# Optimization experiments

Hardware: AMD Instinct MI355X
Metric: run time of the kernel (lower is better)

The kernel has to match this reference:

```python
import jax, jax.numpy as jnp
import numpy as np
from itertools import combinations

# Static config (mirrors args / init_kwargs)
WAY, SHOT, SEQ_LEN, TSS = 5, 16, 10, 2
DIN, DOUT = 2048, 1152
N_QUERIES = 320
TUPLES = np.array(list(combinations(range(SEQ_LEN), TSS)), dtype=np.int32)  # [T, 2]
T = TUPLES.shape[0]  # 45
S = SHOT * T         # support tuples per class
OTHERS = np.array([[o for o in range(WAY) if o != c] for c in range(WAY)], dtype=np.int32)


def _cdist(a, b):
    # Euclidean distance matrix, [Na, Nb]
    d2 = (jnp.sum(a * a, axis=1)[:, None] + jnp.sum(b * b, axis=1)[None, :]
          - 2.0 * a @ b.T)
    return jnp.sqrt(jnp.maximum(d2, 1e-12))


def setup_inputs() -> dict:
    key = jax.random.key(0)
    k1, k2, k3 = jax.random.split(key, 3)
    support_set = jax.random.normal(k1, (WAY * SHOT, SEQ_LEN, DIN), jnp.float32)
    queries = jax.random.normal(k2, (N_QUERIES, SEQ_LEN, DIN), jnp.float32)
    support_labels = jnp.repeat(jnp.arange(WAY, dtype=jnp.int32), SHOT)
    W = jax.random.normal(k3, (DOUT, DIN * TSS), jnp.float32) / np.sqrt(DIN * TSS)
    b = jnp.zeros((DOUT,), jnp.float32)
    return {"support_set": support_set, "queries": queries,
            "support_labels": support_labels, "W": W, "b": b}


def reference(support_set, queries, support_labels, W, b):
    n_q = queries.shape[0]
    # Build frame-pair tuples: [N, T, TSS*DIN]  (dropout is identity in eval)
    sup_t = support_set[:, TUPLES, :].reshape(support_set.shape[0], T, TSS * DIN)
    q_t = queries[:, TUPLES, :].reshape(n_q, T, TSS * DIN)

    q_emb = jax.nn.relu(q_t.reshape(-1, TSS * DIN) @ W.T + b)          # [n_q*T, DOUT]
    order = jnp.argsort(support_labels).reshape(WAY, SHOT)             # class grouping
    class_sup = sup_t[order].reshape(WAY, S, TSS * DIN)
    sup_emb = jax.nn.relu(class_sup @ W.T + b)                          # [WAY, S, DOUT]

    dist_max_c, ave_all_c, pos_all_c = [], [], []
    for c in range(WAY):
        D = _cdist(q_emb, sup_emb[c])                                   # [n_q*T, S]
        # faithful to torch view(-1, T, shot).topk(k=1,dim=1).mean(dim=1)
        ave = D.reshape(-1, T, SHOT).max(axis=1).mean(axis=1)           # [n_q*T]
        dist_max_c.append(D.max(axis=1).reshape(n_q, T).mean(axis=1))   # [n_q]
        ave_all_c.append(ave)
        pos_all_c.append(jnp.argmax(D, axis=1))                         # [n_q*T]
    dist_max = jnp.stack(dist_max_c, axis=1)                            # [n_q, WAY]

    contrast_c = []
    for c in range(WAY):
        mse = sup_emb[c][pos_all_c[c]]                                  # [n_q*T, DOUT]
        so = sup_emb[OTHERS[c]]                                         # [WAY-1, S, DOUT]
        so_flat = so.reshape(-1, DOUT)
        CD = _cdist(mse, so_flat).reshape(-1, WAY - 1, S).transpose(1, 0, 2)  # [WAY-1, n_q*T, S]
        rec = (CD > ave_all_c[c][None, :, None]).sum(axis=1).astype(jnp.float32)  # [WAY-1, S]
        nz = jnp.maximum((rec > 0).sum(axis=1).astype(jnp.float32), 1.0)
        thr = rec.sum(axis=1) / nz
        mask = (rec < thr[:, None]).astype(jnp.float32).reshape(-1)     # [(WAY-1)*S]
        Dd = _cdist(q_emb, so_flat)                                     # [n_q*T, (WAY-1)*S]
        row = (Dd * mask).sum(axis=1) / jnp.maximum(mask.sum(), 1.0)    # masked mean == mean over gathered cols
        contrast_c.append(row.reshape(n_q, T).mean(axis=1) / (WAY - 1))
    dist_contrast = jnp.stack(contrast_c, axis=1)                       # [n_q, WAY]

    dist_sum = dist_contrast + dist_max
    logits_contrast = dist_max / dist_sum
    # (logits_max, logits_contrast) stacked: [2, n_q, WAY]
    return jnp.stack([dist_max, logits_contrast])
```

## Files before the change

### kernel.cpp

```cpp
#include <hip/hip_runtime.h>
#include <hip/hip_bf16.h>
#include <hip/hip_fp16.h>

#define WAY   5
#define SHOT  16
#define TT    45
#define SS    720
#define NQ    320
#define NQT   14400
#define NS    3600
#define MTOT  18000
#define DIN   2048
#define KDIM  4096
#define DOUT  1152
#define EROWS 18176
#define MAXIT 8192

#define QELT  (NQ * 10 * DIN)
#define SELT  (WAY * SHOT * 10 * DIN)
#define WELT  (DOUT * KDIM)

typedef __attribute__((ext_vector_type(8))) short bf16x8;
typedef __attribute__((ext_vector_type(8))) unsigned short u16x8;
typedef __attribute__((ext_vector_type(4))) float f32x4;

#define AS1 __attribute__((address_space(1)))
#define AS3 __attribute__((address_space(3)))

__constant__ unsigned char TUPI[TT] = {
  0,0,0,0,0,0,0,0,0, 1,1,1,1,1,1,1,1, 2,2,2,2,2,2,2,
  3,3,3,3,3,3, 4,4,4,4,4, 5,5,5,5, 6,6,6, 7,7, 8};
__constant__ unsigned char TUPJ[TT] = {
  1,2,3,4,5,6,7,8,9, 2,3,4,5,6,7,8,9, 3,4,5,6,7,8,9,
  4,5,6,7,8,9, 5,6,7,8,9, 6,7,8,9, 7,8,9, 8,9, 9};

__device__ inline unsigned short f2bf(float f) {
  union { float f; unsigned u; } v; v.f = f;
  unsigned r = v.u + 0x7FFFu + ((v.u >> 16) & 1u);
  return (unsigned short)(r >> 16);
}
__device__ inline float bf2f(unsigned short b) {
  union { unsigned u; float f; } v; v.u = ((unsigned)b) << 16;
  return v.f;
}
__device__ inline float h2f(unsigned short h) {
  union { __half h; unsigned short u; } v; v.u = h;
  return __half2float(v.h);
}
__device__ inline unsigned short f2h(float f) {
  union { __half h; unsigned short u; } v; v.h = __float2half(f);
  return v.u;
}

__device__ inline int xcd_swz(int o, int nwg) {
  int q = nwg >> 3, r = nwg & 7;
  int x = o & 7, i = o >> 3;
  return (x < r ? x * (q + 1) : r * (q + 1) + (x - r) * q) + i;
}

__global__ void sentinelK(float* __restrict__ out, float v) {
  int i = blockIdx.x * 256 + threadIdx.x;
  if (i < 2 * NQ * WAY) out[i] = v;
}

__global__ void packK(const float* __restrict__ qry, const float* __restrict__ sup,
                      const float* __restrict__ Wsrc,
                      unsigned short* __restrict__ qbf, unsigned short* __restrict__ sbf,
                      unsigned short* __restrict__ Wbf) {
  long long e = ((long long)blockIdx.x * 256 + threadIdx.x) * 8;
  const float* src; unsigned short* dst; long long o;
  if (e < QELT)                { src = qry;  dst = qbf; o = e; }
  else if (e < QELT + SELT)    { src = sup;  dst = sbf; o = e - QELT; }
  else if (e < QELT + SELT + WELT) { src = Wsrc; dst = Wbf; o = e - QELT - SELT; }
  else return;
  float4 a = *(const float4*)(src + o);
  float4 b = *(const float4*)(src + o + 4);
  u16x8 v;
  v[0] = f2bf(a.x); v[1] = f2bf(a.y); v[2] = f2bf(a.z); v[3] = f2bf(a.w);
  v[4] = f2bf(b.x); v[5] = f2bf(b.y); v[6] = f2bf(b.z); v[7] = f2bf(b.w);
  *(u16x8*)(dst + o) = v;
}

__global__ __launch_bounds__(256) void gemm1K(
    const unsigned short* __restrict__ qbf, const unsigned short* __restrict__ sbf,
    const unsigned short* __restrict__ Wbf, const float* __restrict__ bias,
    unsigned short* __restrict__ emb) {
  __shared__ unsigned short smem[16384];
  unsigned short* Alds = smem;
  unsigned short* Blds = smem + 8192;
  const int tid = threadIdx.x;
  const int lane = tid & 63;
  const int w = tid >> 6, wr = w >> 1, wc = w & 1;
  const int wg = xcd_swz(blockIdx.x, 141 * 9);
  const int bm = wg / 9, bn = wg % 9;

  const unsigned short* pAI[4];
  const unsigned short* pAJ[4];
  const unsigned short* pB[4];
  int ldso[4];
  const int cg8 = ((lane & 7) ^ (lane >> 3)) * 8;
  const unsigned short* Bbase = Wbf + (size_t)bn * 128 * KDIM;
#pragma unroll
  for (int i = 0; i < 4; ++i) {
    int row = w * 32 + i * 8 + (lane >> 3);
    int gr = bm * 128 + row;
    const unsigned short* base; int t;
    if (gr < NQT)       { t = gr % TT; base = qbf + (size_t)(gr / TT) * (10 * DIN); }
    else if (gr < MTOT) { int u = gr - NQT; int c = u / SS; int s = u % SS; t = s % TT;
                          base = sbf + (size_t)(c * SHOT + s / TT) * (10 * DIN); }
    else                { t = 0; base = qbf; }
    pAI[i] = base + (int)TUPI[t] * DIN + cg8;
    pAJ[i] = base + (int)TUPJ[t] * DIN + cg8;
    pB[i]  = Bbase + (size_t)row * KDIM + cg8;
    ldso[i] = __builtin_amdgcn_readfirstlane((w * 32 + i * 8) * 64);
  }
  const int l7 = lane & 7, c2b = lane >> 4;
  const int fo0 = (c2b ^ l7) << 3, fo1 = ((4 | c2b) ^ l7) << 3;
  int aoff[4], boff[4];
#pragma unroll
  for (int m = 0; m < 4; ++m) aoff[m] = (wr * 64 + m * 16 + (lane & 15)) * 64;
#pragma unroll
  for (int n = 0; n < 4; ++n) boff[n] = (wc * 64 + n * 16 + (lane & 15)) * 64;

  f32x4 acc[4][4] = {};

#pragma unroll
  for (int half = 0; half < 2; ++half) {
    const unsigned short* pA0 = half ? pAJ[0] : pAI[0];
    const unsigned short* pA1 = half ? pAJ[1] : pAI[1];
    const unsigned short* pA2 = half ? pAJ[2] : pAI[2];
    const unsigned short* pA3 = half ? pAJ[3] : pAI[3];
    for (int kt2 = 0; kt2 < 32; ++kt2) {
      __builtin_amdgcn_global_load_lds((const AS1 void*)pA0, (AS3 void*)(Alds + ldso[0]), 16, 0, 0); pA0 += 64;
      __builtin_amdgcn_global_load_lds((const AS1 void*)pA1, (AS3 void*)(Alds + ldso[1]), 16, 0, 0); pA1 += 64;
      __builtin_amdgcn_global_load_lds((const AS1 void*)pA2, (AS3 void*)(Alds + ldso[2]), 16, 0, 0); pA2 += 64;
      __builtin_amdgcn_global_load_lds((const AS1 void*)pA3, (AS3 void*)(Alds + ldso[3]), 16, 0, 0); pA3 += 64;
      __builtin_amdgcn_global_load_lds((const AS1 void*)pB[0], (AS3 void*)(Blds + ldso[0]), 16, 0, 0); pB[0] += 64;
      __builtin_amdgcn_global_load_lds((const AS1 void*)pB[1], (AS3 void*)(Blds + ldso[1]), 16, 0, 0); pB[1] += 64;
      __builtin_amdgcn_global_load_lds((const AS1 void*)pB[2], (AS3 void*)(Blds + ldso[2]), 16, 0, 0); pB[2] += 64;
      __builtin_amdgcn_global_load_lds((const AS1 void*)pB[3], (AS3 void*)(Blds + ldso[3]), 16, 0, 0); pB[3] += 64;
      __syncthreads();
#pragma unroll
      for (int kk = 0; kk < 2; ++kk) {
        const int fo = kk ? fo1 : fo0;
        bf16x8 af[4], bfr[4];
#pragma unroll
        for (int m = 0; m < 4; ++m) af[m] = *(const bf16x8*)(&Alds[aoff[m] + fo]);
#pragma unroll
        for (int n = 0; n < 4; ++n) bfr[n] = *(const bf16x8*)(&Blds[boff[n] + fo]);
#pragma unroll
        for (int m = 0; m < 4; ++m)
#pragma unroll
          for (int n = 0; n < 4; ++n)
            acc[m][n] = __builtin_amdgcn_mfma_f32_16x16x32_bf16(af[m], bfr[n], acc[m][n], 0, 0, 0);
      }
      __syncthreads();
    }
  }

  const int lr0 = (lane >> 4) * 4;
  const int lc = lane & 15;
#pragma unroll
  for (int m = 0; m < 4; ++m)
#pragma unroll
    for (int n = 0; n < 4; ++n) {
      int lcol = wc * 64 + n * 16 + lc;
      float bv = bias[bn * 128 + lcol];
#pragma unroll
      for (int q = 0; q < 4; ++q) {
        int lrow = wr * 64 + m * 16 + lr0 + q;
        smem[lrow * 128 + (lcol ^ (((lrow >> 2) & 7) << 4))] =
            f2bf(fmaxf(acc[m][n][q] + bv, 0.0f));
      }
    }
  __syncthreads();
#pragma unroll
  for (int u8i = 0; u8i < 8; ++u8i) {
    int u = u8i * 256 + tid;
    int row = u >> 4, ch = u & 15;
    int gr = bm * 128 + row;
    if (gr < MTOT) {
      u16x8 v = *(const u16x8*)(&smem[row * 128 + ((ch * 8) ^ (((row >> 2) & 7) << 4))]);
      *(u16x8*)(&emb[(size_t)gr * DOUT + bn * 128 + ch * 8]) = v;
    }
  }
}

__global__ __launch_bounds__(256) void gemm2K(
    const unsigned short* __restrict__ emb, const float* __restrict__ norms,
    __half* __restrict__ Dh) {
  __shared__ unsigned short smem[16384];
  unsigned short* Alds = smem;
  unsigned short* Blds = smem + 8192;
  const int tid = threadIdx.x;
  const int lane = tid & 63;
  const int w = tid >> 6, wr = w >> 1, wc = w & 1;
  const int wg = xcd_swz(blockIdx.x, 141 * 29);
  const int bm = wg / 29, bn = wg % 29;

  const unsigned short* pA[4];
  const unsigned short* pB[4];
  int ldso[4];
  const int cg8 = ((lane & 7) ^ (lane >> 3)) * 8;
  const unsigned short* Abase = emb + (size_t)bm * 128 * DOUT;
  const unsigned short* Bbase = emb + (size_t)(NQT + bn * 128) * DOUT;
#pragma unroll
  for (int i = 0; i < 4; ++i) {
    int row = w * 32 + i * 8 + (lane >> 3);
    pA[i] = Abase + (size_t)row * DOUT + cg8;
    pB[i] = Bbase + (size_t)row * DOUT + cg8;
    ldso[i] = __builtin_amdgcn_readfirstlane((w * 32 + i * 8) * 64);
  }
  const int l7 = lane & 7, c2b = lane >> 4;
  const int fo0 = (c2b ^ l7) << 3, fo1 = ((4 | c2b) ^ l7) << 3;
  int aoff[4], boff[4];
#pragma unroll
  for (int m = 0; m < 4; ++m) aoff[m] = (wr * 64 + m * 16 + (lane & 15)) * 64;
#pragma unroll
  for (int n = 0; n < 4; ++n) boff[n] = (wc * 64 + n * 16 + (lane & 15)) * 64;

  f32x4 acc[4][4] = {};

  for (int kt = 0; kt < DOUT / 64; ++kt) {
    __builtin_amdgcn_global_load_lds((const AS1 void*)pA[0], (AS3 void*)(Alds + ldso[0]), 16, 0, 0); pA[0] += 64;
    __builtin_amdgcn_global_load_lds((const AS1 void*)pA[1], (AS3 void*)(Alds + ldso[1]), 16, 0, 0); pA[1] += 64;
    __builtin_amdgcn_global_load_lds((const AS1 void*)pA[2], (AS3 void*)(Alds + ldso[2]), 16, 0, 0); pA[2] += 64;
    __builtin_amdgcn_global_load_lds((const AS1 void*)pA[3], (AS3 void*)(Alds + ldso[3]), 16, 0, 0); pA[3] += 64;
    __builtin_amdgcn_global_load_lds((const AS1 void*)pB[0], (AS3 void*)(Blds + ldso[0]), 16, 0, 0); pB[0] += 64;
    __builtin_amdgcn_global_load_lds((const AS1 void*)pB[1], (AS3 void*)(Blds + ldso[1]), 16, 0, 0); pB[1] += 64;
    __builtin_amdgcn_global_load_lds((const AS1 void*)pB[2], (AS3 void*)(Blds + ldso[2]), 16, 0, 0); pB[2] += 64;
    __builtin_amdgcn_global_load_lds((const AS1 void*)pB[3], (AS3 void*)(Blds + ldso[3]), 16, 0, 0); pB[3] += 64;
    __syncthreads();
#pragma unroll
    for (int kk = 0; kk < 2; ++kk) {
      const int fo = kk ? fo1 : fo0;
      bf16x8 af[4], bfr[4];
#pragma unroll
      for (int m = 0; m < 4; ++m) af[m] = *(const bf16x8*)(&Alds[aoff[m] + fo]);
#pragma unroll
      for (int n = 0; n < 4; ++n) bfr[n] = *(const bf16x8*)(&Blds[boff[n] + fo]);
#pragma unroll
      for (int m = 0; m < 4; ++m)
#pragma unroll
        for (int n = 0; n < 4; ++n)
          acc[m][n] = __builtin_amdgcn_mfma_f32_16x16x32_bf16(af[m], bfr[n], acc[m][n], 0, 0, 0);
    }
    __syncthreads();
  }

  const int lr0 = (lane >> 4) * 4;
  const int lc = lane & 15;
#pragma unroll
  for (int m = 0; m < 4; ++m)
#pragma unroll
    for (int n = 0; n < 4; ++n) {
      int lcol = wc * 64 + n * 16 + lc;
      float nb_ = norms[NQT + bn * 128 + lcol];
#pragma unroll
      for (int q = 0; q < 4; ++q) {
        int lrow = wr * 64 + m * 16 + lr0 + q;
        float d2 = norms[bm * 128 + lrow] + nb_ - 2.0f * acc[m][n][q];
        smem[lrow * 128 + (lcol ^ (((lrow >> 2) & 7) << 4))] =
            f2h(sqrtf(fmaxf(d2, 1e-12f)));
      }
    }
  __syncthreads();
  unsigned short* Dhu = (unsigned short*)Dh;
#pragma unroll
  for (int u8i = 0; u8i < 8; ++u8i) {
    int u = u8i * 256 + tid;
    int row = u >> 4, ch = u & 15;
    int gr = bm * 128 + row;
    int gc0 = bn * 128 + ch * 8;
    if (gr < MTOT && gc0 < NS) {
      u16x8 v = *(const u16x8*)(&smem[row * 128 + ((ch * 8) ^ (((row >> 2) & 7) << 4))]);
      *(u16x8*)(&Dhu[(size_t)gr * NS + gc0]) = v;
    }
  }
}

__global__ void normK(const unsigned short* __restrict__ emb, float* __restrict__ norms) {
  int row = blockIdx.x * 4 + (threadIdx.x >> 6);
  int lane = threadIdx.x & 63;
  const unsigned short* e = emb + (size_t)row * DOUT;
  float acc = 0.f;
  u16x8 x0 = *(const u16x8*)(e + lane * 8);
  u16x8 x1 = *(const u16x8*)(e + 512 + lane * 8);
#pragma unroll
  for (int k = 0; k < 8; ++k) {
    float a = bf2f(x0[k]); acc += a * a;
    float b = bf2f(x1[k]); acc += b * b;
  }
  unsigned t = *(const unsigned*)(e + 1024 + lane * 2);
  float c0 = bf2f((unsigned short)(t & 0xFFFFu)); acc += c0 * c0;
  float c1 = bf2f((unsigned short)(t >> 16));     acc += c1 * c1;
  for (int sh = 1; sh < 64; sh <<= 1) acc += __shfl_xor(acc, sh);
  if (lane == 0) norms[row] = acc;
}

__global__ void passA(const __half* __restrict__ Dh, float* __restrict__ rowmax,
                      float* __restrict__ ave, int* __restrict__ pos) {
  int wid = blockIdx.x * 4 + (threadIdx.x >> 6);
  int lane = threadIdx.x & 63;
  int c = wid / NQT, r = wid % NQT;
  const unsigned short* row = (const unsigned short*)(Dh + (size_t)r * NS + c * SS);
  u16x8 v0 = *(const u16x8*)(row + lane * 8);
  bool act1 = lane < 26;
  u16x8 v1 = v0;
  if (act1) v1 = *(const u16x8*)(row + 512 + lane * 8);
  float m8[8];
  unsigned pm = 0;
#pragma unroll
  for (int k = 0; k < 8; ++k) {
    unsigned h0 = v0[k];
    int col0 = lane * 8 + k;
    unsigned p0 = (h0 << 16) | (unsigned)(65535 - col0);
    pm = pm > p0 ? pm : p0;
    m8[k] = h2f((unsigned short)h0);
  }
  if (act1) {
#pragma unroll
    for (int k = 0; k < 8; ++k) {
      unsigned h1 = v1[k];
      int col1 = 512 + lane * 8 + k;
      unsigned p1 = (h1 << 16) | (unsigned)(65535 - col1);
      pm = pm > p1 ? pm : p1;
      m8[k] = fmaxf(m8[k], h2f((unsigned short)h1));
    }
  }
  for (int sh = 1; sh < 64; sh <<= 1) {
    unsigned o = (unsigned)__shfl_xor((int)pm, sh);
    pm = pm > o ? pm : o;
  }
  for (int sh = 2; sh < 64; sh <<= 1) {
#pragma unroll
    for (int k = 0; k < 8; ++k)
      m8[k] = fmaxf(m8[k], __shfl_xor(m8[k], sh));
  }
  float sj = ((m8[0] + m8[1]) + (m8[2] + m8[3])) + ((m8[4] + m8[5]) + (m8[6] + m8[7]));
  sj += __shfl_xor(sj, 1);
  if (lane == 0) {
    rowmax[c * NQT + r] = h2f((unsigned short)(pm >> 16));
    ave[c * NQT + r] = sj * (1.0f / 16.0f);
    pos[c * NQT + r] = 65535 - (int)(pm & 0xFFFFu);
  }
}

__global__ void bucketCntK(const int* __restrict__ pos, unsigned* __restrict__ bcnt) {
  __shared__ unsigned h[NS];
  int tid = threadIdx.x;
  for (int i = tid; i < NS; i += 256) h[i] = 0;
  __syncthreads();
  for (int idx = blockIdx.x * 256 + tid; idx < WAY * NQT; idx += gridDim.x * 256) {
    int c = idx / NQT;
    atomicAdd(&h[c * SS + pos[idx]], 1u);
  }
  __syncthreads();
  for (int i = tid; i < NS; i += 256) {
    unsigned v = h[i];
    if (v) atomicAdd(&bcnt[i], v);
  }
}

__global__ void pfxItemsK(const unsigned* __restrict__ bcnt, unsigned* __restrict__ bstart,
                          unsigned* __restrict__ nitems, unsigned* __restrict__ items) {
  __shared__ unsigned s[1024];
  int c = blockIdx.x, tid = threadIdx.x;
  for (int i = tid; i < 1024; i += 256) s[i] = (i < SS) ? bcnt[c * SS + i] : 0u;
  __syncthreads();
  for (int off = 1; off < 1024; off <<= 1) {
    unsigned v[4];
#pragma unroll
    for (int k = 0; k < 4; ++k) { int i = tid + k * 256; v[k] = (i >= off) ? s[i - off] : 0u; }
    __syncthreads();
#pragma unroll
    for (int k = 0; k < 4; ++k) { int i = tid + k * 256; s[i] += v[k]; }
    __syncthreads();
  }
  for (int i = tid; i < SS; i += 256) {
    unsigned excl = (i ? s[i - 1] : 0u);
    bstart[c * SS + i] = excl;
    unsigned nb = s[i] - excl;
    if (nb) {
      unsigned ni = (nb + 63) >> 6;
      unsigned base = atomicAdd(nitems, ni);
      for (unsigned k = 0; k < ni; ++k) items[base + k] = ((unsigned)(c * SS + i) << 8) | k;
    }
  }
}

__global__ void bucketSctK(const int* __restrict__ pos, const float* __restrict__ ave,
                           const unsigned* __restrict__ bstart, unsigned* __restrict__ bfill,
                           float* __restrict__ bav) {
  int idx = blockIdx.x * 256 + threadIdx.x;
  if (idx >= WAY * NQT) return;
  int c = idx / NQT;
  int p = pos[idx];
  unsigned j = atomicAdd(&bfill[c * SS + p], 1u);
  bav[c * NQT + bstart[c * SS + p] + j] = ave[idx];
}

__global__ __launch_bounds__(256) void recK4(const __half* __restrict__ Dh,
                                             const unsigned* __restrict__ bstart,
                                             const unsigned* __restrict__ bcnt,
                                             const float* __restrict__ bav,
                                             const unsigned* __restrict__ items,
                                             const unsigned* __restrict__ nitems,
                                             unsigned* __restrict__ rec) {
  int lane = threadIdx.x & 63, wv = threadIdx.x >> 6;
  int nit = (int)nitems[0];
  int nw = gridDim.x * 4;
  for (int i = blockIdx.x * 4 + wv; i < nit; i += nw) {
    unsigned it = items[i];
    int cp = (int)(it >> 8), k = (int)(it & 255u);
    int c = cp / SS, p = cp % SS;
    int c0 = c * SS;
    int b0 = (int)bstart[cp], nb = (int)bcnt[cp];
    int j0 = k << 6;
    float av = (j0 + lane < nb) ? bav[c * NQT + b0 + j0 + lane] : 3.0e38f;
    const __half* row = Dh + (size_t)(NQT + c0 + p) * NS;
    for (int itr = 0; itr < 45; ++itr) {
      int os = itr * 64 + lane;
      int col = os + ((os >= c0) ? SS : 0);
      float v = __half2float(row[col]);
      unsigned cnt = 0;
#pragma unroll 16
      for (int j = 0; j < 64; ++j)
        cnt += (v > __shfl(av, j)) ? 1u : 0u;
      if (cnt) atomicAdd(&rec[c * 2880 + os], cnt);
    }
  }
}

__global__ void maskK(const unsigned* __restrict__ rec, float* __restrict__ maskfull,
                      float* __restrict__ nmask) {
  int c = blockIdx.x;
  int tid = threadIdx.x, lane = tid & 63, wv = tid >> 6;
  __shared__ float thr[WAY - 1];
  __shared__ float red[8];
  for (int o = 0; o < WAY - 1; ++o) {
    float s = 0.f, nz = 0.f;
    for (int i = tid; i < SS; i += 256) {
      unsigned v = rec[c * (WAY - 1) * SS + o * SS + i];
      s += (float)v;
      if (v > 0u) nz += 1.f;
    }
    for (int sh = 1; sh < 64; sh <<= 1) { s += __shfl_xor(s, sh); nz += __shfl_xor(nz, sh); }
    if (lane == 0) { red[wv] = s; red[4 + wv] = nz; }
    __syncthreads();
    if (tid == 0) thr[o] = (red[0] + red[1] + red[2] + red[3]) /
                           fmaxf(red[4] + red[5] + red[6] + red[7], 1.0f);
    __syncthreads();
  }
  float cntm = 0.f;
  for (int col = tid; col < NS; col += 256) {
    float mv = 0.f;
    int cb = col / SS;
    if (cb != c) {
      int os = col - ((col >= (c + 1) * SS) ? SS : 0);
      mv = (((float)rec[c * (WAY - 1) * SS + os]) < thr[os / SS]) ? 1.f : 0.f;
    }
    maskfull[c * NS + col] = mv;
    cntm += mv;
  }
  for (int sh = 1; sh < 64; sh <<= 1) cntm += __shfl_xor(cntm, sh);
  if (lane == 0) red[wv] = cntm;
  __syncthreads();
  if (tid == 0) nmask[c] = red[0] + red[1] + red[2] + red[3];
}

__global__ void mask5K(const float* __restrict__ maskfull, unsigned char* __restrict__ mask5) {
  int col = blockIdx.x * 256 + threadIdx.x;
  if (col >= NS) return;
  unsigned m = 0;
#pragma unroll
  for (int c = 0; c < WAY; ++c)
    m |= (maskfull[c * NS + col] > 0.5f) ? (1u << c) : 0u;
  mask5[col] = (unsigned char)m;
}

__global__ void passB(const __half* __restrict__ Dh, const unsigned char* __restrict__ mask5,
                      const float* __restrict__ nmask, float* __restrict__ row5) {
  int r = blockIdx.x * 4 + (threadIdx.x >> 6);
  int lane = threadIdx.x & 63;
  const unsigned short* drow = (const unsigned short*)(Dh + (size_t)r * NS);
  float a[WAY] = {0.f, 0.f, 0.f, 0.f, 0.f};
#pragma unroll
  for (int it = 0; it < 8; ++it) {
    int col = it * 512 + lane * 8;
    if (col < NS) {
      u16x8 v = *(const u16x8*)(drow + col);
      unsigned long long mb = *(const unsigned long long*)(mask5 + col);
#pragma unroll
      for (int k = 0; k < 8; ++k) {
        float f = h2f(v[k]);
        unsigned m = (unsigned)(mb >> (8 * k)) & 31u;
#pragma unroll
        for (int c = 0; c < WAY; ++c) a[c] += ((m >> c) & 1u) ? f : 0.f;
      }
    }
  }
#pragma unroll
  for (int c = 0; c < WAY; ++c)
    for (int sh = 1; sh < 64; sh <<= 1) a[c] += __shfl_xor(a[c], sh);
  if (lane == 0)
#pragma unroll
    for (int c = 0; c < WAY; ++c)
      row5[(size_t)r * WAY + c] = a[c] / fmaxf(nmask[c], 1.0f);
}

__global__ void finalK(const float* __restrict__ rowmax, const float* __restrict__ row5,
                       float* __restrict__ out) {
  int idx = blockIdx.x * 256 + threadIdx.x;
  if (idx >= NQ * WAY) return;
  int q = idx / WAY, c = idx % WAY;
  float sm = 0.f, sc = 0.f;
  for (int t = 0; t < TT; ++t) {
    int r = q * TT + t;
    sm += rowmax[c * NQT + r];
    sc += row5[(size_t)r * WAY + c];
  }
  float dm = sm / 45.0f;
  float ctr = sc / 45.0f * 0.25f;
  out[idx] = dm;
  out[NQ * WAY + idx] = dm / (ctr + dm);
}

extern "C" void kernel_launch(void* const* d_in, const int* in_sizes, int n_in,
                              void* d_out, int out_size, void* d_ws, size_t ws_size,
                              hipStream_t stream) {
  const float* sup  = (const float*)d_in[0];
  const float* qry  = (const float*)d_in[1];
  const float* Wsrc = (const float*)d_in[3];
  const float* bias = (const float*)d_in[4];
  float* out = (float*)d_out;

  char* base = (char*)d_ws;
  size_t off = 0;
  __half* Dh = (__half*)(base + off);                  off += (size_t)MTOT * NS * 2;
  unsigned short* qbf = (unsigned short*)Dh;
  unsigned short* sbf = qbf + QELT;
  unsigned short* Wbf = sbf + SELT;
  unsigned short* emb = (unsigned short*)(base + off); off += (size_t)EROWS * DOUT * 2;
  float* norms  = (float*)(base + off);   off += (size_t)EROWS * 4;
  float* rowmax = (float*)(base + off);   off += (size_t)WAY * NQT * 4;
  float* ave    = (float*)(base + off);   off += (size_t)WAY * NQT * 4;
  int*   pos    = (int*)(base + off);     off += (size_t)WAY * NQT * 4;
  char* zbase = base + off;
  unsigned* rec    = (unsigned*)(base + off); off += (size_t)WAY * (WAY - 1) * SS * 4;
  unsigned* bcnt   = (unsigned*)(base + off); off += (size_t)WAY * SS * 4;
  unsigned* bfill  = (unsigned*)(base + off); off += (size_t)WAY * SS * 4;
  unsigned* nitems = (unsigned*)(base + off); off += 64;
  size_t zbytes = (size_t)((base + off) - zbase);
  unsigned* bstart = (unsigned*)(base + off); off += (size_t)WAY * SS * 4;
  float* maskfull = (float*)(base + off); off += (size_t)WAY * NS * 4;
  unsigned char* mask5 = (unsigned char*)(base + off); off += 4096;
  float* nmask  = (float*)(base + off);   off += 64;
  float* row5   = (float*)(base + off);   off += (size_t)NQT * WAY * 4;
  float* bav    = (float*)(base + off);   off += (size_t)WAY * NQT * 4;
  unsigned* items = (unsigned*)(base + off); off += MAXIT * 4;

  if (ws_size < off) {
    sentinelK<<<13, 256, 0, stream>>>(out, -(1000.0f + (float)(ws_size >> 20)));
    return;
  }

  (void)hipMemsetAsync(zbase, 0, zbytes, stream);
  packK<<<6304, 256, 0, stream>>>(qry, sup, Wsrc, qbf, sbf, Wbf);
  gemm1K<<<141 * 9, 256, 0, stream>>>(qbf, sbf, Wbf, bias, emb);
  normK<<<4500, 256, 0, stream>>>(emb, norms);
  gemm2K<<<141 * 29, 256, 0, stream>>>(emb, norms, Dh);
  passA<<<18000, 256, 0, stream>>>(Dh, rowmax, ave, pos);
  bucketCntK<<<282, 256, 0, stream>>>(pos, bcnt);
  pfxItemsK<<<WAY, 256, 0, stream>>>(bcnt, bstart, nitems, items);
  bucketSctK<<<282, 256, 0, stream>>>(pos, ave, bstart, bfill, bav);
  recK4<<<1184, 256, 0, stream>>>(Dh, bstart, bcnt, bav, items, nitems, rec);
  maskK<<<WAY, 256, 0, stream>>>(rec, maskfull, nmask);
  mask5K<<<15, 256, 0, stream>>>(maskfull, mask5);
  passB<<<3600, 256, 0, stream>>>(Dh, mask5, nmask, row5);
  finalK<<<7, 256, 0, stream>>>(rowmax, row5, out);
}
```

Before: 628.4 us.

## Double-buffer LDS tiles in distance GEMM to overlap loads with MFMA

The gemm2K distance kernel now keeps two LDS buffers, so each k-step's global-to-LDS loads go into the other buffer while MFMAs read the current one. The goal is to hide global memory latency behind compute and drop one barrier per iteration. In exchange, LDS use per block doubles to 64KB, which can lower occupancy. The epilogue still reuses the start of smem after a final barrier.

```diff
diff --git a/kernel.cpp b/kernel.cpp
--- a/kernel.cpp
+++ b/kernel.cpp
@@ -189,9 +189,7 @@
 __global__ __launch_bounds__(256) void gemm2K(
     const unsigned short* __restrict__ emb, const float* __restrict__ norms,
     __half* __restrict__ Dh) {
-  __shared__ unsigned short smem[16384];
-  unsigned short* Alds = smem;
-  unsigned short* Blds = smem + 8192;
+  __shared__ unsigned short smem[32768];
   const int tid = threadIdx.x;
   const int lane = tid & 63;
   const int w = tid >> 6, wr = w >> 1, wc = w & 1;
@@ -221,32 +219,48 @@
 
   f32x4 acc[4][4] = {};
 
-  for (int kt = 0; kt < DOUT / 64; ++kt) {
-    __builtin_amdgcn_global_load_lds((const AS1 void*)pA[0], (AS3 void*)(Alds + ldso[0]), 16, 0, 0); pA[0] += 64;
-    __builtin_amdgcn_global_load_lds((const AS1 void*)pA[1], (AS3 void*)(Alds + ldso[1]), 16, 0, 0); pA[1] += 64;
-    __builtin_amdgcn_global_load_lds((const AS1 void*)pA[2], (AS3 void*)(Alds + ldso[2]), 16, 0, 0); pA[2] += 64;
-    __builtin_amdgcn_global_load_lds((const AS1 void*)pA[3], (AS3 void*)(Alds + ldso[3]), 16, 0, 0); pA[3] += 64;
-    __builtin_amdgcn_global_load_lds((const AS1 void*)pB[0], (AS3 void*)(Blds + ldso[0]), 16, 0, 0); pB[0] += 64;
-    __builtin_amdgcn_global_load_lds((const AS1 void*)pB[1], (AS3 void*)(Blds + ldso[1]), 16, 0, 0); pB[1] += 64;
-    __builtin_amdgcn_global_load_lds((const AS1 void*)pB[2], (AS3 void*)(Blds + ldso[2]), 16, 0, 0); pB[2] += 64;
-    __builtin_amdgcn_global_load_lds((const AS1 void*)pB[3], (AS3 void*)(Blds + ldso[3]), 16, 0, 0); pB[3] += 64;
-    __syncthreads();
+  auto stage = [&](int buf) {
+    unsigned short* ab = smem + (buf << 14);
+    unsigned short* bb = ab + 8192;
+    __builtin_amdgcn_global_load_lds((const AS1 void*)pA[0], (AS3 void*)(ab + ldso[0]), 16, 0, 0); pA[0] += 64;
+    __builtin_amdgcn_global_load_lds((const AS1 void*)pA[1], (AS3 void*)(ab + ldso[1]), 16, 0, 0); pA[1] += 64;
+    __builtin_amdgcn_global_load_lds((const AS1 void*)pA[2], (AS3 void*)(ab + ldso[2]), 16, 0, 0); pA[2] += 64;
+    __builtin_amdgcn_global_load_lds((const AS1 void*)pA[3], (AS3 void*)(ab + ldso[3]), 16, 0, 0); pA[3] += 64;
+    __builtin_amdgcn_global_load_lds((const AS1 void*)pB[0], (AS3 void*)(bb + ldso[0]), 16, 0, 0); pB[0] += 64;
+    __builtin_amdgcn_global_load_lds((const AS1 void*)pB[1], (AS3 void*)(bb + ldso[1]), 16, 0, 0); pB[1] += 64;
+    __builtin_amdgcn_global_load_lds((const AS1 void*)pB[2], (AS3 void*)(bb + ldso[2]), 16, 0, 0); pB[2] += 64;
+    __builtin_amdgcn_global_load_lds((const AS1 void*)pB[3], (AS3 void*)(bb + ldso[3]), 16, 0, 0); pB[3] += 64;
+  };
+  auto compute = [&](int buf) {
+    const unsigned short* ca = smem + (buf << 14);
+    const unsigned short* cb = ca + 8192;
 #pragma unroll
     for (int kk = 0; kk < 2; ++kk) {
       const int fo = kk ? fo1 : fo0;
       bf16x8 af[4], bfr[4];
 #pragma unroll
-      for (int m = 0; m < 4; ++m) af[m] = *(const bf16x8*)(&Alds[aoff[m] + fo]);
-#pragma unroll
-      for (int n = 0; n < 4; ++n) bfr[n] = *(const bf16x8*)(&Blds[boff[n] + fo]);
+      for (int m = 0; m < 4; ++m) af[m] = *(const bf16x8*)(&ca[aoff[m] + fo]);
+#pragma unroll
+      for (int n = 0; n < 4; ++n) bfr[n] = *(const bf16x8*)(&cb[boff[n] + fo]);
 #pragma unroll
       for (int m = 0; m < 4; ++m)
 #pragma unroll
         for (int n = 0; n < 4; ++n)
           acc[m][n] = __builtin_amdgcn_mfma_f32_16x16x32_bf16(af[m], bfr[n], acc[m][n], 0, 0, 0);
     }
+  };
+
+  stage(0);
+  __syncthreads();
+  int cur = 0;
+  for (int kt = 0; kt < DOUT / 64 - 1; ++kt) {
+    stage(cur ^ 1);
+    compute(cur);
     __syncthreads();
-  }
+    cur ^= 1;
+  }
+  compute(cur);
+  __syncthreads();
 
   const int lr0 = (lane >> 4) * 4;
   const int lc = lane & 15;
```

Result: no change. 622.7 us (-0.9%).
